# Performance work log

Measured on AMD Instinct MI355X. Metric: run time of the kernel, lower is better.

## Reference

```python
import jax, jax.numpy as jnp
import numpy as np

B, S, HID = 2, 2048, 2048
H, KV, D = 16, 8, 128          # query heads, kv heads, head_dim
EPS = 1e-6
THETA = 1000000.0


def setup_inputs() -> dict:
    key = jax.random.key(0)
    ks = jax.random.split(key, 8)
    sc = 0.02
    hidden_states = jax.random.normal(ks[0], (B, S, HID), dtype=jnp.float32)
    Wq = jax.random.normal(ks[1], (HID, H * D), dtype=jnp.float32) * sc
    Wk = jax.random.normal(ks[2], (HID, KV * D), dtype=jnp.float32) * sc
    Wv = jax.random.normal(ks[3], (HID, KV * D), dtype=jnp.float32) * sc
    Wo = jax.random.normal(ks[4], (H * D, HID), dtype=jnp.float32) * sc
    q_norm_w = jnp.ones((D,), dtype=jnp.float32)
    k_norm_w = jnp.ones((D,), dtype=jnp.float32)
    positions = jnp.arange(S, dtype=jnp.int32)
    # causal mask: True = masked (j > i)
    attention_mask = jnp.triu(jnp.ones((S, S), dtype=bool), k=1)
    return {
        "hidden_states": hidden_states, "Wq": Wq, "Wk": Wk, "Wv": Wv,
        "Wo": Wo, "q_norm_w": q_norm_w, "k_norm_w": k_norm_w,
        "positions": positions, "attention_mask": attention_mask,
    }


def _rms_norm(x, w):
    # x: [..., D]; RMSNorm over last dim
    var = jnp.mean(x * x, axis=-1, keepdims=True)
    return x * jax.lax.rsqrt(var + EPS) * w


def _rope(x, positions):
    # x: [B, h, S, D]; standard rotate-half RoPE
    inv_freq = 1.0 / (THETA ** (jnp.arange(0, D, 2, dtype=jnp.float32) / D))
    ang = positions.astype(jnp.float32)[:, None] * inv_freq[None, :]  # [S, D/2]
    cos = jnp.concatenate([jnp.cos(ang), jnp.cos(ang)], axis=-1)      # [S, D]
    sin = jnp.concatenate([jnp.sin(ang), jnp.sin(ang)], axis=-1)
    x1, x2 = x[..., : D // 2], x[..., D // 2:]
    rot = jnp.concatenate([-x2, x1], axis=-1)
    return x * cos + rot * sin


def reference(hidden_states, Wq, Wk, Wv, Wo, q_norm_w, k_norm_w,
              positions, attention_mask):
    b, s, _ = hidden_states.shape
    q = (hidden_states @ Wq).reshape(b, s, H, D).transpose(0, 2, 1, 3)   # [B,H,S,D]
    k = (hidden_states @ Wk).reshape(b, s, KV, D).transpose(0, 2, 1, 3)  # [B,KV,S,D]
    v = (hidden_states @ Wv).reshape(b, s, KV, D).transpose(0, 2, 1, 3)
    q = _rms_norm(q, q_norm_w)
    k = _rms_norm(k, k_norm_w)
    q = _rope(q, positions)
    k = _rope(k, positions)
    # GQA: repeat kv heads
    g = H // KV
    k = jnp.repeat(k, g, axis=1)  # [B,H,S,D]
    v = jnp.repeat(v, g, axis=1)
    scale = 1.0 / np.sqrt(D).astype(np.float32)
    scores = jnp.einsum('bhqd,bhkd->bhqk', q, k) * scale
    scores = jnp.where(attention_mask[None, None, :, :], -jnp.inf, scores)
    attn = jax.nn.softmax(scores, axis=-1)
    out = jnp.einsum('bhqk,bhkd->bhqd', attn, v)
    out = out.transpose(0, 2, 1, 3).reshape(b, s, H * D)
    return out @ Wo
```

## Files before the change

### kernel.cpp

```cpp
#include <hip/hip_runtime.h>
#include <hip/hip_bf16.h>

typedef __hip_bfloat16 bf16;
typedef __attribute__((ext_vector_type(8))) short short8v;
typedef __attribute__((ext_vector_type(4))) float f32x4;

constexpr int nB = 2;
constexpr int nS = 2048;
constexpr int nHID = 2048;
constexpr int nH = 16;
constexpr int nKV = 8;
constexpr int nD = 128;
constexpr int QS = 4096;
constexpr float kEps = 1e-6f;
constexpr float kScale = 0.08838834764831845f;

template <int N>
struct IC {
  static constexpr int value = N;
};

__device__ inline float b2f(unsigned short u) {
  return __uint_as_float(((unsigned)u) << 16);
}
__device__ inline float bf2f(bf16 v) { return __bfloat162float(v); }
__device__ inline short f2bs(float f) {
  bf16 h = __float2bfloat16(f);
  return *reinterpret_cast<short*>(&h);
}
__device__ inline unsigned pack2bf(float a, float b) {
  return ((unsigned)(unsigned short)f2bs(b) << 16) |
         (unsigned)(unsigned short)f2bs(a);
}

__device__ inline void gload_lds16(const bf16* g, bf16* l) {
  __builtin_amdgcn_global_load_lds(
      (const __attribute__((address_space(1))) void*)g,
      (__attribute__((address_space(3))) void*)l, 16, 0, 0);
}

template <int N>
__device__ inline void vwait() {
  asm volatile("s_waitcnt vmcnt(%0)" ::"n"(N) : "memory");
}

__global__ __launch_bounds__(256) void preproc(
    const float* __restrict__ hs, const float* __restrict__ Wq,
    const float* __restrict__ Wk, const float* __restrict__ Wv,
    const float* __restrict__ Wo, bf16* __restrict__ hsb,
    bf16* __restrict__ Wcat, bf16* __restrict__ Wot,
    float2* __restrict__ tab) {
  int t = blockIdx.x;
  if (t < 12288) {
    const float* src;
    bf16* dst;
    int N;
    if (t < 4096) {
      src = Wq; dst = Wcat; N = 2048;
    } else if (t < 6144) {
      t -= 4096; src = Wk; dst = Wcat + (size_t)2048 * 2048; N = 1024;
    } else if (t < 8192) {
      t -= 6144; src = Wv; dst = Wcat + (size_t)3072 * 2048; N = 1024;
    } else {
      t -= 8192; src = Wo; dst = Wot; N = 2048;
    }
    const int tilesN = N >> 5;
    const int n0 = (t % tilesN) * 32, k0 = (t / tilesN) * 32;
    __shared__ float tb[32][33];
    const int c = threadIdx.x & 31, r8 = threadIdx.x >> 5;
#pragma unroll
    for (int i = 0; i < 4; ++i)
      tb[r8 + i * 8][c] = src[(size_t)(k0 + r8 + i * 8) * N + n0 + c];
    __syncthreads();
#pragma unroll
    for (int i = 0; i < 4; ++i)
      dst[(size_t)(n0 + r8 + i * 8) * 2048 + k0 + c] =
          __float2bfloat16(tb[c][r8 + i * 8]);
  } else if (t < 20480) {
    const int i = ((t - 12288) * 256 + threadIdx.x) * 4;
    const float4 v = *reinterpret_cast<const float4*>(hs + i);
    ushort4 o;
    o.x = (unsigned short)f2bs(v.x);
    o.y = (unsigned short)f2bs(v.y);
    o.z = (unsigned short)f2bs(v.z);
    o.w = (unsigned short)f2bs(v.w);
    *reinterpret_cast<ushort4*>(hsb + i) = o;
  } else {
    const int idx = (t - 20480) * 256 + threadIdx.x;
    const int s = idx >> 6, j = idx & 63;
    const float invf = expf(-(float)j * (13.815510557964274f / 64.0f));
    const float ang = (float)s * invf;
    tab[idx] = make_float2(cosf(ang), sinf(ang));
  }
}

template <int BM, int BN, typename OUT_T>
__global__ __launch_bounds__(512) void gemm_8ph(
    const bf16* __restrict__ A, const bf16* __restrict__ Bt,
    OUT_T* __restrict__ C, int M, int N, int K) {
  constexpr int LA = BM / 128;
  constexpr int LB = BN / 128;
  constexpr int MF = BM / 32;
  constexpr int MFH = MF / 2;
  constexpr int NF = BN / 64;
  constexpr int W = 2 * (LA + LB);
  constexpr int LDSB = 2 * BM * 32 + 2 * BN * 32;
  __shared__ bf16 lds[2 * LDSB];

  const int tid = threadIdx.x;
  const int wave = tid >> 6, lane = tid & 63;
  const int lr = lane & 15, lg = lane >> 4;
  const int wm = wave >> 2, wn = wave & 3;
  const int m0 = blockIdx.y * BM, n0 = blockIdx.x * BN;
  const int srow = tid >> 2;
  const int scol = (((tid & 3) ^ ((tid >> 3) & 3)) << 3);
  const int fsw = (lr >> 1) & 3;

  auto stageA = [&](int t, int kk) {
    bf16* dst = lds + (t & 1) * LDSB + kk * (BM * 32) + wave * 512;
    const bf16* src = A + (size_t)(m0 + srow) * K + t * 64 + kk * 32 + scol;
#pragma unroll
    for (int j = 0; j < LA; ++j)
      gload_lds16(src + (size_t)(j * 128) * K, dst + j * 4096);
  };
  auto stageB = [&](int t, int kk) {
    bf16* dst =
        lds + (t & 1) * LDSB + 2 * BM * 32 + kk * (BN * 32) + wave * 512;
    const bf16* src = Bt + (size_t)(n0 + srow) * K + t * 64 + kk * 32 + scol;
#pragma unroll
    for (int j = 0; j < LB; ++j)
      gload_lds16(src + (size_t)(j * 128) * K, dst + j * 4096);
  };

  f32x4 acc[MF][NF];
#pragma unroll
  for (int m = 0; m < MF; ++m)
#pragma unroll
    for (int n = 0; n < NF; ++n) acc[m][n] = (f32x4){0.f, 0.f, 0.f, 0.f};
  short8v bfr[NF];

  auto phase = [&](auto WC, int buf, int kk, int mh, auto stageFn) {
    constexpr int WAIT = decltype(WC)::value;
    if constexpr (WAIT >= 0) vwait<WAIT>();
    __builtin_amdgcn_s_barrier();
    asm volatile("" ::: "memory");
    if (mh == 0) {
      const bf16* bb = lds + buf * LDSB + 2 * BM * 32 + kk * (BN * 32);
#pragma unroll
      for (int ni = 0; ni < NF; ++ni)
        bfr[ni] = *reinterpret_cast<const short8v*>(
            bb + (wn * (BN / 4) + ni * 16 + lr) * 32 + ((lg ^ fsw) << 3));
    }
    short8v af[MFH];
    const bf16* ab = lds + buf * LDSB + kk * (BM * 32);
#pragma unroll
    for (int ii = 0; ii < MFH; ++ii)
      af[ii] = *reinterpret_cast<const short8v*>(
          ab + (wm * (BM / 2) + (mh * MFH + ii) * 16 + lr) * 32 +
          ((lg ^ fsw) << 3));
    stageFn();
    asm volatile("s_waitcnt lgkmcnt(0)" ::: "memory");
    __builtin_amdgcn_sched_barrier(0);
    __builtin_amdgcn_s_setprio(1);
#pragma unroll
    for (int ii = 0; ii < MFH; ++ii)
#pragma unroll
      for (int ni = 0; ni < NF; ++ni)
        acc[mh * MFH + ii][ni] = __builtin_amdgcn_mfma_f32_16x16x32_bf16(
            af[ii], bfr[ni], acc[mh * MFH + ii][ni], 0, 0, 0);
    __builtin_amdgcn_s_setprio(0);
  };

  const int NT = K / 64;
  stageA(0, 0);
  stageB(0, 0);
  stageA(0, 1);
  stageB(0, 1);
  stageA(1, 0);
  stageB(1, 0);

  for (int t = 0; t < NT - 1; ++t) {
    const int buf = t & 1;
    phase(IC<W>{}, buf, 0, 0, [&] { stageA(t + 1, 1); });
    phase(IC<-1>{}, buf, 0, 1, [&] { stageB(t + 1, 1); });
    phase(IC<W>{}, buf, 1, 0, [&] {
      if (t < NT - 2) stageA(t + 2, 0);
    });
    phase(IC<-1>{}, buf, 1, 1, [&] {
      if (t < NT - 2) stageB(t + 2, 0);
    });
  }
  {
    const int buf = (NT - 1) & 1;
    phase(IC<LA + LB>{}, buf, 0, 0, [&] {});
    phase(IC<-1>{}, buf, 0, 1, [&] {});
    phase(IC<0>{}, buf, 1, 0, [&] {});
    phase(IC<-1>{}, buf, 1, 1, [&] {});
  }

#pragma unroll
  for (int m = 0; m < MF; ++m)
#pragma unroll
    for (int n = 0; n < NF; ++n)
#pragma unroll
      for (int r = 0; r < 4; ++r) {
        const int row = m0 + wm * (BM / 2) + m * 16 + 4 * lg + r;
        const int col = n0 + wn * (BN / 4) + n * 16 + lr;
        if constexpr (sizeof(OUT_T) == 2)
          C[(size_t)row * N + col] = __float2bfloat16(acc[m][n][r]);
        else
          C[(size_t)row * N + col] = acc[m][n][r];
      }
}

__global__ __launch_bounds__(256) void norm_rope_k(
    bf16* __restrict__ qkv, const float* __restrict__ kw,
    const float2* __restrict__ tab) {
  const int row = blockIdx.x;
  const int g = threadIdx.x >> 7;
  const int t = threadIdx.x & 127;
  const int head = blockIdx.y * 2 + g;
  const int s = row & (nS - 1);
  bf16* xp = qkv + (size_t)row * QS + 2048 + head * nD;
  const float v = bf2f(xp[t]);
  float ss = v * v;
#pragma unroll
  for (int off = 32; off > 0; off >>= 1) ss += __shfl_xor(ss, off);
  __shared__ float wsum[2][2];
  __shared__ float buf[2][nD];
  if ((t & 63) == 0) wsum[g][t >> 6] = ss;
  __syncthreads();
  const float inv = rsqrtf((wsum[g][0] + wsum[g][1]) * (1.0f / nD) + kEps);
  const float nv = v * inv * kw[t];
  buf[g][t] = nv;
  __syncthreads();
  const float partner = buf[g][t ^ 64];
  const float rot = (t < 64) ? -partner : partner;
  const int j = t & 63;
  const float2 cs = tab[s * 64 + j];
  const float outv = nv * cs.x + rot * cs.y;
  xp[t] = __float2bfloat16(outv);
}

constexpr int BQ = 128, BKT = 64;

__global__ __launch_bounds__(512) void attn_mfma(
    const bf16* __restrict__ QKV, bf16* __restrict__ O,
    const float* __restrict__ qw, const float2* __restrict__ tab) {
  const int l = blockIdx.x;
  const int bh = l & 31;
  const int rr0 = l >> 5;
  const int qb = (rr0 < 8) ? 15 - rr0 : rr0 - 8;
  const int b = bh >> 4, h = bh & 15, kvh = h >> 1;
  const int q0 = qb * BQ;
  const int nt = 2 * qb + 2;
  const int tid = threadIdx.x;
  const int wave = tid >> 6, lane = tid & 63;
  const int lr = lane & 15, lg = lane >> 4;

  __shared__ bf16 Ks[BKT][136];
  __shared__ bf16 Vt[nD][72];
  __shared__ bf16 Pl[8][16][72];

  const bf16* Qbase = QKV + (size_t)b * nS * QS + h * nD;
  const bf16* Kbase = QKV + (size_t)b * nS * QS + 2048 + kvh * nD;
  const bf16* Vbase = QKV + (size_t)b * nS * QS + 3072 + kvh * nD;

  const int krow = tid >> 3, kcc = (tid & 7) * 16;
  const int vkey = tid & 63, vdc = (tid >> 6) * 16;

  short8v kreg[2], vreg[2];
  auto gload = [&](int kt) {
    const bf16* ksrc = Kbase + (size_t)(kt + krow) * QS + kcc;
    const bf16* vsrc = Vbase + (size_t)(kt + vkey) * QS + vdc;
    kreg[0] = *reinterpret_cast<const short8v*>(ksrc);
    kreg[1] = *reinterpret_cast<const short8v*>(ksrc + 8);
    vreg[0] = *reinterpret_cast<const short8v*>(vsrc);
    vreg[1] = *reinterpret_cast<const short8v*>(vsrc + 8);
  };
  auto lwrite = [&]() {
    *reinterpret_cast<short8v*>(&Ks[krow][kcc]) = kreg[0];
    *reinterpret_cast<short8v*>(&Ks[krow][kcc + 8]) = kreg[1];
#pragma unroll
    for (int i = 0; i < 2; ++i)
#pragma unroll
      for (int j = 0; j < 8; ++j)
        *reinterpret_cast<short*>(&Vt[vdc + 8 * i + j][vkey]) = vreg[i][j];
  };

  short8v qf[4];
  {
    const int qrow_i = q0 + 16 * wave + lr;
    const bf16* qrow = Qbase + (size_t)qrow_i * QS;
    float x[4][8];
    float ss = 0.f;
#pragma unroll
    for (int dc = 0; dc < 4; ++dc) {
      const short8v raw =
          *reinterpret_cast<const short8v*>(qrow + 32 * dc + 8 * lg);
#pragma unroll
      for (int j2 = 0; j2 < 8; ++j2) {
        const float v = b2f((unsigned short)raw[j2]);
        x[dc][j2] = v;
        ss += v * v;
      }
    }
    ss += __shfl_xor(ss, 16);
    ss += __shfl_xor(ss, 32);
    const float inv = rsqrtf(ss * (1.0f / nD) + kEps);
#pragma unroll
    for (int dc = 0; dc < 4; ++dc) {
      const float4 w0 = *reinterpret_cast<const float4*>(qw + 32 * dc + 8 * lg);
      const float4 w1 =
          *reinterpret_cast<const float4*>(qw + 32 * dc + 8 * lg + 4);
      const float wv[8] = {w0.x, w0.y, w0.z, w0.w, w1.x, w1.y, w1.z, w1.w};
#pragma unroll
      for (int j2 = 0; j2 < 8; ++j2) x[dc][j2] *= inv * wv[j2];
    }
#pragma unroll
    for (int dc = 0; dc < 4; ++dc) {
      short8v q8;
#pragma unroll
      for (int j2 = 0; j2 < 8; ++j2) {
        const int c = 32 * dc + 8 * lg + j2;
        const float2 cs = tab[qrow_i * 64 + (c & 63)];
        const float rot = (dc < 2) ? -x[dc ^ 2][j2] : x[dc ^ 2][j2];
        q8[j2] = f2bs(x[dc][j2] * cs.x + rot * cs.y);
      }
      qf[dc] = q8;
    }
  }

  f32x4 of[8];
#pragma unroll
  for (int n = 0; n < 8; ++n) of[n] = (f32x4){0.f, 0.f, 0.f, 0.f};
  float m_run = -1e30f, l_run = 0.f;

  gload(0);
  lwrite();
  __syncthreads();

  for (int j = 0; j < nt; ++j) {
    const int kt = j * BKT;
    const bool have_next = (j + 1 < nt);
    if (have_next) gload((j + 1) * BKT);

    f32x4 s[4];
    __builtin_amdgcn_s_setprio(1);
#pragma unroll
    for (int sub = 0; sub < 4; ++sub) {
      f32x4 acc = {0.f, 0.f, 0.f, 0.f};
#pragma unroll
      for (int dc = 0; dc < 4; ++dc) {
        const short8v kf = *reinterpret_cast<const short8v*>(
            &Ks[16 * sub + lr][32 * dc + 8 * lg]);
        acc = __builtin_amdgcn_mfma_f32_16x16x32_bf16(kf, qf[dc], acc, 0, 0, 0);
      }
      s[sub] = acc;
    }
    __builtin_amdgcn_s_setprio(0);

    const bool needMask = (kt + BKT > q0 + 16 * wave);
#pragma unroll
    for (int sub = 0; sub < 4; ++sub)
#pragma unroll
      for (int r = 0; r < 4; ++r) {
        float v = s[sub][r] * kScale;
        if (needMask && (kt + 16 * sub + 4 * lg + r > q0 + 16 * wave + lr))
          v = -1e30f;
        s[sub][r] = v;
      }

    float pmax = -1e30f;
#pragma unroll
    for (int sub = 0; sub < 4; ++sub)
#pragma unroll
      for (int r = 0; r < 4; ++r) pmax = fmaxf(pmax, s[sub][r]);
    pmax = fmaxf(pmax, __shfl_xor(pmax, 16));
    pmax = fmaxf(pmax, __shfl_xor(pmax, 32));

    if (!__all(pmax - m_run <= 8.f)) {
      const float mt = fmaxf(m_run, pmax);
      const float corr = __expf(m_run - mt);
#pragma unroll
      for (int n = 0; n < 8; ++n) of[n] *= corr;
      l_run *= corr;
      m_run = mt;
    }

    float p[4][4];
    float lsum = 0.f;
#pragma unroll
    for (int sub = 0; sub < 4; ++sub)
#pragma unroll
      for (int r = 0; r < 4; ++r) {
        const float e = __expf(s[sub][r] - m_run);
        p[sub][r] = e;
        lsum += e;
      }
    lsum += __shfl_xor(lsum, 16);
    lsum += __shfl_xor(lsum, 32);
    l_run += lsum;

#pragma unroll
    for (int sub = 0; sub < 4; ++sub)
#pragma unroll
      for (int rp = 0; rp < 2; ++rp)
        *reinterpret_cast<unsigned*>(
            &Pl[wave][lr][16 * sub + 4 * lg + 2 * rp]) =
            pack2bf(p[sub][2 * rp], p[sub][2 * rp + 1]);

    __builtin_amdgcn_s_setprio(1);
#pragma unroll
    for (int kk = 0; kk < 2; ++kk) {
      const short8v pb =
          *reinterpret_cast<const short8v*>(&Pl[wave][lr][32 * kk + 8 * lg]);
#pragma unroll
      for (int n = 0; n < 8; ++n) {
        const short8v vf = *reinterpret_cast<const short8v*>(
            &Vt[16 * n + lr][32 * kk + 8 * lg]);
        of[n] = __builtin_amdgcn_mfma_f32_16x16x32_bf16(vf, pb, of[n], 0, 0, 0);
      }
    }
    __builtin_amdgcn_s_setprio(0);

    if (have_next) {
      __syncthreads();
      lwrite();
      __syncthreads();
    }
  }

  {
    const float inv = 1.0f / l_run;
    bf16* orow = O + ((size_t)(b * nS + q0 + 16 * wave + lr)) * (nH * nD) +
                 h * nD + 4 * lg;
#pragma unroll
    for (int n = 0; n < 8; ++n)
#pragma unroll
      for (int rp = 0; rp < 2; ++rp)
        *reinterpret_cast<unsigned*>(orow + 16 * n + 2 * rp) =
            pack2bf(of[n][2 * rp] * inv, of[n][2 * rp + 1] * inv);
  }
}

extern "C" void kernel_launch(void* const* d_in, const int* in_sizes, int n_in,
                              void* d_out, int out_size, void* d_ws,
                              size_t ws_size, hipStream_t stream) {
  const float* hs = (const float*)d_in[0];
  const float* Wq = (const float*)d_in[1];
  const float* Wk = (const float*)d_in[2];
  const float* Wv = (const float*)d_in[3];
  const float* Wo = (const float*)d_in[4];
  const float* qw = (const float*)d_in[5];
  const float* kw = (const float*)d_in[6];

  const int M = nB * nS;
  char* ws = (char*)d_ws;
  size_t off = 0;
  auto alloc = [&](size_t bytes) {
    char* p = ws + off;
    off += bytes;
    return p;
  };
  bf16* hsb = (bf16*)alloc((size_t)M * nHID * 2);
  bf16* att = hsb;
  bf16* qkv = (bf16*)alloc((size_t)M * QS * 2);
  bf16* Wcat = (bf16*)alloc((size_t)QS * nHID * 2);
  bf16* Wot = (bf16*)alloc((size_t)nH * nD * nHID * 2);
  float2* tab = (float2*)alloc((size_t)nS * 64 * 8);
  float* out = (float*)d_out;

  preproc<<<dim3(20992), 256, 0, stream>>>(hs, Wq, Wk, Wv, Wo, hsb, Wcat, Wot,
                                           tab);

  gemm_8ph<256, 256, bf16><<<dim3(QS / 256, M / 256), 512, 0, stream>>>(
      hsb, Wcat, qkv, M, QS, nHID);

  norm_rope_k<<<dim3(M, nKV / 2), 256, 0, stream>>>(qkv, kw, tab);

  attn_mfma<<<dim3(512), 512, 0, stream>>>(qkv, att, qw, tab);

  gemm_8ph<128, 256, float><<<dim3(nHID / 256, M / 128), 512, 0, stream>>>(
      att, Wot, out, M, nHID, nH * nD);
}
```

Measured before the change: 219.8 us.

## Fuse K RMSNorm and RoPE into QKV GEMM epilogue

Removes the separate norm_rope_k kernel and applies K-head RMSNorm and RoPE in the epilogue of the QKV projection GEMM, for blocks covering the K columns. Row sums of squares are reduced across lanes and across wave pairs through LDS, and rotate-half partners are exchanged through LDS. This saves a kernel launch and a read-modify-write pass over the K slice of qkv. The cost is extra syncs and epilogue work in those GEMM blocks, plus a bf16 rounding of the partner value.

```diff
diff --git a/kernel.cpp b/kernel.cpp
--- a/kernel.cpp
+++ b/kernel.cpp
@@ -94,10 +94,11 @@
   }
 }
 
-template <int BM, int BN, typename OUT_T>
+template <int BM, int BN, bool KNORM, typename OUT_T>
 __global__ __launch_bounds__(512) void gemm_8ph(
     const bf16* __restrict__ A, const bf16* __restrict__ Bt,
-    OUT_T* __restrict__ C, int M, int N, int K) {
+    OUT_T* __restrict__ C, int M, int N, int K,
+    const float* __restrict__ kw, const float2* __restrict__ tab) {
   constexpr int LA = BM / 128;
   constexpr int LB = BN / 128;
   constexpr int MF = BM / 32;
@@ -198,6 +199,86 @@
     phase(IC<-1>{}, buf, 1, 1, [&] {});
   }
 
+  if constexpr (KNORM) {
+    if (blockIdx.x >= 8 && blockIdx.x < 12) {
+      float ps[MF][4];
+#pragma unroll
+      for (int m = 0; m < MF; ++m)
+#pragma unroll
+        for (int r = 0; r < 4; ++r) {
+          float s2 = 0.f;
+#pragma unroll
+          for (int n = 0; n < NF; ++n) s2 += acc[m][n][r] * acc[m][n][r];
+#pragma unroll
+          for (int off = 1; off < 16; off <<= 1) s2 += __shfl_xor(s2, off);
+          ps[m][r] = s2;
+        }
+      float* sums = reinterpret_cast<float*>(lds);
+      __syncthreads();
+      if (lr == 0) {
+#pragma unroll
+        for (int m = 0; m < MF; ++m)
+#pragma unroll
+          for (int r = 0; r < 4; ++r)
+            sums[wn * 256 + wm * 128 + m * 16 + 4 * lg + r] = ps[m][r];
+      }
+      __syncthreads();
+      float inv[MF][4];
+#pragma unroll
+      for (int m = 0; m < MF; ++m)
+#pragma unroll
+        for (int r = 0; r < 4; ++r) {
+          const int rp = wm * 128 + m * 16 + 4 * lg + r;
+          const float tot = sums[wn * 256 + rp] + sums[(wn ^ 1) * 256 + rp];
+          inv[m][r] = rsqrtf(tot * (1.0f / nD) + kEps);
+        }
+      __syncthreads();
+      bf16* ex = lds;
+      const int colbase = (wn & 1) * 64;
+      float kwl[NF];
+#pragma unroll
+      for (int n = 0; n < NF; ++n) kwl[n] = kw[colbase + n * 16 + lr];
+      const int pw = wave ^ 1;
+      for (int half = 0; half < 2; ++half) {
+#pragma unroll
+        for (int m = 0; m < MF; ++m)
+#pragma unroll
+          for (int nn = 0; nn < 2; ++nn) {
+            const int n = 2 * half + nn;
+#pragma unroll
+            for (int r = 0; r < 4; ++r) {
+              const float nv = acc[m][n][r] * inv[m][r] * kwl[n];
+              ex[(wave * 128 + m * 16 + 4 * lg + r) * 36 + nn * 16 + lr] =
+                  __float2bfloat16(nv);
+            }
+          }
+        __syncthreads();
+#pragma unroll
+        for (int m = 0; m < MF; ++m)
+#pragma unroll
+          for (int nn = 0; nn < 2; ++nn) {
+            const int n = 2 * half + nn;
+#pragma unroll
+            for (int r = 0; r < 4; ++r) {
+              const int row = m0 + wm * 128 + m * 16 + 4 * lg + r;
+              const int s = row & (nS - 1);
+              const int c = colbase + n * 16 + lr;
+              const float nv = acc[m][n][r] * inv[m][r] * kwl[n];
+              const float partner = bf2f(
+                  ex[(pw * 128 + m * 16 + 4 * lg + r) * 36 + nn * 16 + lr]);
+              const float rot = (c < 64) ? -partner : partner;
+              const float2 cs = tab[s * 64 + (c & 63)];
+              const int col = n0 + wn * 64 + n * 16 + lr;
+              C[(size_t)row * N + col] =
+                  __float2bfloat16(nv * cs.x + rot * cs.y);
+            }
+          }
+        __syncthreads();
+      }
+      return;
+    }
+  }
+
 #pragma unroll
   for (int m = 0; m < MF; ++m)
 #pragma unroll
@@ -211,35 +292,6 @@
         else
           C[(size_t)row * N + col] = acc[m][n][r];
       }
-}
-
-__global__ __launch_bounds__(256) void norm_rope_k(
-    bf16* __restrict__ qkv, const float* __restrict__ kw,
-    const float2* __restrict__ tab) {
-  const int row = blockIdx.x;
-  const int g = threadIdx.x >> 7;
-  const int t = threadIdx.x & 127;
-  const int head = blockIdx.y * 2 + g;
-  const int s = row & (nS - 1);
-  bf16* xp = qkv + (size_t)row * QS + 2048 + head * nD;
-  const float v = bf2f(xp[t]);
-  float ss = v * v;
-#pragma unroll
-  for (int off = 32; off > 0; off >>= 1) ss += __shfl_xor(ss, off);
-  __shared__ float wsum[2][2];
-  __shared__ float buf[2][nD];
-  if ((t & 63) == 0) wsum[g][t >> 6] = ss;
-  __syncthreads();
-  const float inv = rsqrtf((wsum[g][0] + wsum[g][1]) * (1.0f / nD) + kEps);
-  const float nv = v * inv * kw[t];
-  buf[g][t] = nv;
-  __syncthreads();
-  const float partner = buf[g][t ^ 64];
-  const float rot = (t < 64) ? -partner : partner;
-  const int j = t & 63;
-  const float2 cs = tab[s * 64 + j];
-  const float outv = nv * cs.x + rot * cs.y;
-  xp[t] = __float2bfloat16(outv);
 }
 
 constexpr int BQ = 128, BKT = 64;
@@ -474,13 +526,13 @@
   preproc<<<dim3(20992), 256, 0, stream>>>(hs, Wq, Wk, Wv, Wo, hsb, Wcat, Wot,
                                            tab);
 
-  gemm_8ph<256, 256, bf16><<<dim3(QS / 256, M / 256), 512, 0, stream>>>(
-      hsb, Wcat, qkv, M, QS, nHID);
-
-  norm_rope_k<<<dim3(M, nKV / 2), 256, 0, stream>>>(qkv, kw, tab);
+  gemm_8ph<256, 256, true, bf16><<<dim3(QS / 256, M / 256), 512, 0, stream>>>(
+      hsb, Wcat, qkv, M, QS, nHID, kw, tab);
 
   attn_mfma<<<dim3(512), 512, 0, stream>>>(qkv, att, qw, tab);
 
-  gemm_8ph<128, 256, float><<<dim3(nHID / 256, M / 128), 512, 0, stream>>>(
-      att, Wot, out, M, nHID, nH * nD);
-}
+  gemm_8ph<128, 256, false, float>
+      <<<dim3(nHID / 256, M / 128), 512, 0, stream>>>(att, Wot, out, M, nHID,
+                                                      nH * nD, nullptr,
+                                                      nullptr);
+}
```

Measured after the change: 224.1 us. About the same (+2.0%).
